# Kernel optimization log

Hardware: AMD Instinct MI355X
Metric: run time of the kernel (lower is better)

The kernel has to match this reference:

```python
import jax, jax.numpy as jnp
import numpy as np
import math

H = 16
SEG = 128
DIL = 2


def hilbert_perm(M: int) -> jnp.ndarray:
    # Boustrophedon (snake) traversal of a ceil(sqrt(M)) grid, matching
    # create_hilbert_mapping_simple: skip linear positions >= M, keep first M.
    g = int(math.ceil(math.sqrt(M)))
    grid = np.arange(g * g).reshape(g, g)
    grid[1::2] = grid[1::2, ::-1]
    flat = grid.reshape(-1)
    flat = flat[flat < M][:M]
    return jnp.asarray(flat, dtype=jnp.int32)


def setup_inputs() -> dict:
    key = jax.random.key(0)
    kx, kq, ko = jax.random.split(key, 3)
    B, M, D = 4, 4096, 1024
    x = jax.random.normal(kx, (B, M, D), dtype=jnp.float32)
    # nn.Linear weights: [out_features, in_features], y = x @ W.T
    w_qkv = jax.random.normal(kq, (3 * D, D), dtype=jnp.float32) * (D ** -0.5)
    w_out = jax.random.normal(ko, (D, D), dtype=jnp.float32) * (D ** -0.5)
    return {"x": x, "w_qkv": w_qkv, "w_out": w_out}


def reference(x, w_qkv, w_out):
    B, M, Dm = x.shape
    hd = Dm // H
    scale = hd ** -0.5
    S = M // SEG  # number of segments (M chosen as a multiple of SEG)

    qkv = x @ w_qkv.T                              # [B, M, 3*Dm]
    qkv = qkv.reshape(B, M, 3, H, hd)
    q = qkv[:, :, 0].transpose(0, 2, 1, 3)         # [B, H, M, hd]
    k = qkv[:, :, 1].transpose(0, 2, 1, 3)
    v = qkv[:, :, 2].transpose(0, 2, 1, 3)

    perm = hilbert_perm(M)
    qh = q[:, :, perm]                             # Hilbert-reordered
    kh = k[:, :, perm]
    vh = v[:, :, perm]

    # segment-local dilated attention: each query attends to keys at
    # positions seg_start + j*DIL within its own segment
    qh = qh.reshape(B, H, S, SEG, hd)
    kd = kh.reshape(B, H, S, SEG, hd)[:, :, :, ::DIL]   # [B,H,S,SEG//DIL,hd]
    vd = vh.reshape(B, H, S, SEG, hd)[:, :, :, ::DIL]

    scores = jnp.einsum('bhsqd,bhskd->bhsqk', qh * scale, kd)
    attn = jax.nn.softmax(scores, axis=-1)
    o = jnp.einsum('bhsqk,bhskd->bhsqd', attn, vd)       # [B,H,S,SEG,hd]
    o = o.reshape(B, H, M, hd).transpose(0, 2, 1, 3).reshape(B, M, Dm)
    return o @ w_out.T
```

## Files before the change

### kernel.cpp

```cpp
#include <hip/hip_runtime.h>


typedef _Float16 f16x8 __attribute__((ext_vector_type(8)));
typedef _Float16 f16x4 __attribute__((ext_vector_type(4)));
typedef float f32x4 __attribute__((ext_vector_type(4)));

__device__ __forceinline__ int hperm(int i) {
  int r = i >> 6, c = i & 63;
  return (r << 6) | ((r & 1) ? (63 - c) : c);
}
__device__ __forceinline__ int arow_gather(int mp) {
  int b = mp >> 11, i = mp & 2047;
  int s = i >> 6, j = i & 63;
  return b * 4096 + hperm(s * 128 + 2 * j);
}
__device__ __forceinline__ void gload_lds16(const _Float16* g, _Float16* l) {
  __builtin_amdgcn_global_load_lds(
      (const __attribute__((address_space(1))) void*)g,
      (__attribute__((address_space(3))) void*)l, 16, 0, 0);
}

__global__ __launch_bounds__(256) void cast_all(
    const float* __restrict__ x, _Float16* __restrict__ xh,
    const float* __restrict__ wq, _Float16* __restrict__ wqh,
    const float* __restrict__ wo, _Float16* __restrict__ woh) {
  for (int i = blockIdx.x * 256 + threadIdx.x; i < 5242880; i += 256 * 2048) {
    const float* s;
    _Float16* d;
    int j;
    if (i < 4194304) {
      s = x; d = xh; j = i;
    } else if (i < 4980736) {
      s = wq; d = wqh; j = i - 4194304;
    } else {
      s = wo; d = woh; j = i - 4980736;
    }
    float4 v = ((const float4*)s)[j];
    f16x4 o;
    o[0] = (_Float16)v.x;
    o[1] = (_Float16)v.y;
    o[2] = (_Float16)v.z;
    o[3] = (_Float16)v.w;
    *(f16x4*)&d[(size_t)j * 4] = o;
  }
}

#define BAR __builtin_amdgcn_s_barrier()
#define SB0 __builtin_amdgcn_sched_barrier(0)
#define LGKM_(n)                                                  \
  do {                                                            \
    asm volatile("s_waitcnt lgkmcnt(" #n ")" ::: "memory");       \
    SB0;                                                          \
  } while (0)
#define VM4 asm volatile("s_waitcnt vmcnt(4)" ::: "memory")
#define VM2 asm volatile("s_waitcnt vmcnt(2)" ::: "memory")
#define VM0 asm volatile("s_waitcnt vmcnt(0)" ::: "memory")
#define VMX

#define RDA(dst, bi, ks)                                       \
  _Pragma("unroll") for (int m = 0; m < 4; m++) dst[ks][m] =   \
      *(const f16x8*)(aRd[bi][ks] + m * 1024);
#define RDB(dst, bi, q)                                                     \
  _Pragma("unroll") for (int ks = 0; ks < 2; ks++)                          \
      _Pragma("unroll") for (int nf = 0; nf < 2; nf++) dst[ks][nf] =        \
          *(const f16x8*)(bRd[bi][ks] + (q)*2048 + nf * 1024);

#define SA(kt, buf, h)                                                        \
  do {                                                                        \
    gload_lds16(Ab + aOff[(h)*2] + (kt)*64, &lds[buf][0][(h)*8192 + t8]);     \
    gload_lds16(Ab + aOff[(h)*2 + 1] + (kt)*64,                               \
                &lds[buf][0][(h)*8192 + 4096 + t8]);                          \
  } while (0)
#define SBt(kt, buf, h)                                                       \
  do {                                                                        \
    gload_lds16(Bb + bOff[(h)*2] + (kt)*64, &lds[buf][1][(h)*8192 + t8]);     \
    gload_lds16(Bb + bOff[(h)*2 + 1] + (kt)*64,                               \
                &lds[buf][1][(h)*8192 + 4096 + t8]);                          \
  } while (0)

#define MMQ(AC, BS, q)                                                      \
  __builtin_amdgcn_s_setprio(1);                                            \
  _Pragma("unroll") for (int m = 0; m < 4; m++)                             \
      _Pragma("unroll") for (int nf = 0; nf < 2; nf++)                      \
          _Pragma("unroll") for (int ks = 0; ks < 2; ks++) acc[m][2 * (q) + \
                                                               nf] =        \
              __builtin_amdgcn_mfma_f32_16x16x32_f16(                       \
                  AC[ks][m], BS[ks][nf], acc[m][2 * (q) + nf], 0, 0, 0);    \
  __builtin_amdgcn_s_setprio(0);

#define KT(P, T, RD_A, S1, S2, S3, VQ2, VQ3, RD_B0, AN, AC, LGA, LGB3) \
  do {                                                                 \
                                                               \
    if (RD_A) { RDA(AN, (P) ^ 1, 0); }                                 \
    RDB(bS1, (P), 1);                                                  \
    if (S1) { SBt((T) + 1, (P) ^ 1, 1); }                              \
    BAR; LGKM_(LGA); MMQ(AC, bS0, 0);                                  \
                                                               \
    if (RD_A) { RDA(AN, (P) ^ 1, 1); }                                 \
    RDB(bS0, (P), 2);                                                  \
    if (S2) { SA((T) + 2, (P), 0); }                                   \
    BAR; LGKM_(LGA); MMQ(AC, bS1, 1);                                  \
                                                               \
    RDB(bS1, (P), 3);                                                  \
    if (S2) { SA((T) + 2, (P), 1); }                                   \
    VQ2; BAR; LGKM_(4); MMQ(AC, bS0, 2);                               \
                                                               \
    if (RD_B0) { RDB(bS0, (P) ^ 1, 0); }                               \
    if (S3) { SBt((T) + 2, (P), 0); }                                  \
    VQ3; BAR; LGKM_(LGB3); MMQ(AC, bS1, 3);                            \
  } while (0)

template <typename OutT>
__device__ __forceinline__ void gemm_body(
    const _Float16* __restrict__ Ab, const _Float16* __restrict__ Bb,
    const unsigned* aOff, const unsigned* bOff, OutT* __restrict__ C, int N,
    size_t arow0, size_t bcol0, _Float16 (&lds)[2][2][16384]) {
  const int t = threadIdx.x;
  const int lane = t & 63, wave = t >> 6;
  const int wm = wave >> 1, wn = wave & 1;
  const int lr = lane & 15, lg = lane >> 4;
  const int t8 = t * 8;

  const int cx0 = (lg * 8) ^ ((lr & 7) << 3);
  const int cx1 = cx0 ^ 32;
  const _Float16* aRd[2][2];
  const _Float16* bRd[2][2];
#pragma unroll
  for (int bf = 0; bf < 2; bf++) {
    aRd[bf][0] = &lds[bf][0][(wm * 64 + lr) * 64 + cx0];
    aRd[bf][1] = &lds[bf][0][(wm * 64 + lr) * 64 + cx1];
    bRd[bf][0] = &lds[bf][1][(wn * 128 + lr) * 64 + cx0];
    bRd[bf][1] = &lds[bf][1][(wn * 128 + lr) * 64 + cx1];
  }

  f32x4 acc[4][8] = {};
  f16x8 aEv[2][4], aOd[2][4], bS0[2][2], bS1[2][2];

  SA(0, 0, 0); SA(0, 0, 1); SBt(0, 0, 0); SBt(0, 0, 1);
  SA(1, 1, 0); SA(1, 1, 1);
  VM4;
  BAR;
  RDA(aEv, 0, 0); RDA(aEv, 0, 1); RDB(bS0, 0, 0);
  SBt(1, 1, 0);
  VM2;
  BAR;

  for (int i = 0; i < 7; i++) {
    KT(0, 2 * i,     1, 1, 1, 1, VM4, VM2, 1, aOd, aEv, 8, 4);
    KT(1, 2 * i + 1, 1, 1, 1, 1, VM4, VM2, 1, aEv, aOd, 8, 4);
  }
  KT(0, 14, 1, 1, 0, 0, VM0, VMX, 1, aOd, aEv, 8, 4);
  KT(1, 15, 0, 0, 0, 0, VMX, VMX, 0, aEv, aOd, 4, 0);

#pragma unroll
  for (int m = 0; m < 4; m++) {
    size_t row0 = arow0 + wm * 64 + m * 16 + lg * 4;
#pragma unroll
    for (int n = 0; n < 8; n++) {
      size_t col = bcol0 + wn * 128 + (n >> 1) * 32 + (n & 1) * 16 + lr;
#pragma unroll
      for (int j = 0; j < 4; j++)
        C[(row0 + j) * N + col] = (OutT)acc[m][n][j];
    }
  }
}

__global__ __launch_bounds__(512, 2) void gemm_qkv(
    const _Float16* __restrict__ xh, const _Float16* __restrict__ wqh,
    _Float16* __restrict__ qh, _Float16* __restrict__ kvh) {
  __shared__ _Float16 lds[2][2][16384];
  const int t = threadIdx.x;
  const int id = blockIdx.x;
  const int sw = (id & 7) * (gridDim.x >> 3) + (id >> 3);
  const bool iskv = sw >= 256;
  const int wid = iskv ? sw - 256 : sw;
  const int N = iskv ? 2048 : 1024;
  const int bn = iskv ? (wid & 7) : (wid & 3);
  const int bm = iskv ? (wid >> 3) : (wid >> 2);
  const _Float16* Bb = wqh + (iskv ? (size_t)1048576 : 0);
  _Float16* C = iskv ? kvh : qh;

  const int sgrow = t >> 3;
  const int sgcol = ((t & 7) * 8) ^ ((sgrow & 7) << 3);
  unsigned aOff[4], bOff[4];
#pragma unroll
  for (int r = 0; r < 4; r++) {
    int mr = bm * 256 + 64 * r + sgrow;
    int ar = iskv ? arow_gather(mr) : mr;
    aOff[r] = (unsigned)ar * 1024u + (unsigned)sgcol;
    bOff[r] = ((unsigned)(bn * 256 + 64 * r + sgrow)) * 1024u + (unsigned)sgcol;
  }
  gemm_body<_Float16>(xh, Bb, aOff, bOff, C, N, (size_t)bm * 256,
                      (size_t)bn * 256, lds);
}

__global__ __launch_bounds__(512, 2) void gemm_out(
    const _Float16* __restrict__ atth, const _Float16* __restrict__ woh,
    float* __restrict__ out) {
  __shared__ _Float16 lds[2][2][16384];
  const int t = threadIdx.x;
  const int id = blockIdx.x;
  const int sw = (id & 7) * (gridDim.x >> 3) + (id >> 3);
  const int bn = sw & 3, bm = sw >> 2;

  const int sgrow = t >> 3;
  const int sgcol = ((t & 7) * 8) ^ ((sgrow & 7) << 3);
  unsigned aOff[4], bOff[4];
#pragma unroll
  for (int r = 0; r < 4; r++) {
    aOff[r] = ((unsigned)(bm * 256 + 64 * r + sgrow)) * 1024u + (unsigned)sgcol;
    bOff[r] = ((unsigned)(bn * 256 + 64 * r + sgrow)) * 1024u + (unsigned)sgcol;
  }
  gemm_body<float>(atth, woh, aOff, bOff, out, 1024, (size_t)bm * 256,
                   (size_t)bn * 256, lds);
}

#define STRD 72

__global__ __launch_bounds__(256) void hilbert_attn(
    const _Float16* __restrict__ qh, const _Float16* __restrict__ kvh,
    _Float16* __restrict__ aout) {
  __shared__ _Float16 Qs[128 * STRD];
  __shared__ _Float16 Ks[64 * STRD];
  __shared__ _Float16 Vt[64 * STRD];
  __shared__ _Float16 Ps[128 * STRD];
  const int blk = blockIdx.x;
  const int s = blk & 31, h = (blk >> 5) & 15, b = blk >> 9;
  const int t = threadIdx.x, lane = t & 63, wave = t >> 6;
  const int lr = lane & 15, lg = lane >> 4, lk = lg * 8;
  const int col = (t & 7) * 8, rr = t >> 3;
  const size_t kvb = ((size_t)b * 2048 + s * 64) * 2048;

#pragma unroll
  for (int i = 0; i < 4; i++) {
    int m = i * 32 + rr;
    int p = b * 4096 + hperm(s * 128 + m);
    *(f16x8*)&Qs[m * STRD + col] =
        *(const f16x8*)&qh[(size_t)p * 1024 + h * 64 + col];
  }
#pragma unroll
  for (int i = 0; i < 2; i++) {
    int j = i * 32 + rr;
    *(f16x8*)&Ks[j * STRD + col] =
        *(const f16x8*)&kvh[kvb + (size_t)j * 2048 + h * 64 + col];
    f16x8 vv =
        *(const f16x8*)&kvh[kvb + (size_t)j * 2048 + 1024 + h * 64 + col];
#pragma unroll
    for (int e = 0; e < 8; e++) Vt[(col + e) * STRD + j] = vv[e];
  }
  __syncthreads();

  f32x4 accs[2][4] = {};
#pragma unroll
  for (int kk = 0; kk < 2; kk++) {
    f16x8 aa[2], bb[4];
#pragma unroll
    for (int m = 0; m < 2; m++)
      aa[m] = *(const f16x8*)&Qs[(wave * 32 + m * 16 + lr) * STRD + kk * 32 + lk];
#pragma unroll
    for (int n = 0; n < 4; n++)
      bb[n] = *(const f16x8*)&Ks[(n * 16 + lr) * STRD + kk * 32 + lk];
#pragma unroll
    for (int m = 0; m < 2; m++)
#pragma unroll
      for (int n = 0; n < 4; n++)
        accs[m][n] =
            __builtin_amdgcn_mfma_f32_16x16x32_f16(aa[m], bb[n], accs[m][n], 0, 0, 0);
  }

#pragma unroll
  for (int m = 0; m < 2; m++) {
#pragma unroll
    for (int j = 0; j < 4; j++) {
      float sc0 = accs[m][0][j] * 0.125f;
      float sc1 = accs[m][1][j] * 0.125f;
      float sc2 = accs[m][2][j] * 0.125f;
      float sc3 = accs[m][3][j] * 0.125f;
      float mx = fmaxf(fmaxf(sc0, sc1), fmaxf(sc2, sc3));
#pragma unroll
      for (int d = 1; d < 16; d <<= 1) mx = fmaxf(mx, __shfl_xor(mx, d, 16));
      float e0 = __expf(sc0 - mx), e1 = __expf(sc1 - mx);
      float e2 = __expf(sc2 - mx), e3 = __expf(sc3 - mx);
      float sum = (e0 + e1) + (e2 + e3);
#pragma unroll
      for (int d = 1; d < 16; d <<= 1) sum += __shfl_xor(sum, d, 16);
      float inv = 1.0f / sum;
      int row = wave * 32 + m * 16 + lg * 4 + j;
      Ps[row * STRD + 0 * 16 + lr] = (_Float16)(e0 * inv);
      Ps[row * STRD + 1 * 16 + lr] = (_Float16)(e1 * inv);
      Ps[row * STRD + 2 * 16 + lr] = (_Float16)(e2 * inv);
      Ps[row * STRD + 3 * 16 + lr] = (_Float16)(e3 * inv);
    }
  }
  __syncthreads();

  f32x4 acco[2][4] = {};
#pragma unroll
  for (int kk = 0; kk < 2; kk++) {
    f16x8 aa[2], bb[4];
#pragma unroll
    for (int m = 0; m < 2; m++)
      aa[m] = *(const f16x8*)&Ps[(wave * 32 + m * 16 + lr) * STRD + kk * 32 + lk];
#pragma unroll
    for (int n = 0; n < 4; n++)
      bb[n] = *(const f16x8*)&Vt[(n * 16 + lr) * STRD + kk * 32 + lk];
#pragma unroll
    for (int m = 0; m < 2; m++)
#pragma unroll
      for (int n = 0; n < 4; n++)
        acco[m][n] =
            __builtin_amdgcn_mfma_f32_16x16x32_f16(aa[m], bb[n], acco[m][n], 0, 0, 0);
  }

  const size_t orow0 = (size_t)b * 4096 + s * 128;
#pragma unroll
  for (int m = 0; m < 2; m++) {
#pragma unroll
    for (int n = 0; n < 4; n++) {
#pragma unroll
      for (int j = 0; j < 4; j++) {
        size_t row = orow0 + wave * 32 + m * 16 + lg * 4 + j;
        aout[row * 1024 + h * 64 + n * 16 + lr] = (_Float16)acco[m][n][j];
      }
    }
  }
}

extern "C" void kernel_launch(void* const* d_in, const int* in_sizes, int n_in,
                              void* d_out, int out_size, void* d_ws, size_t ws_size,
                              hipStream_t stream) {
  const float* x = (const float*)d_in[0];
  const float* w_qkv = (const float*)d_in[1];
  const float* w_out = (const float*)d_in[2];
  float* out = (float*)d_out;
  char* ws = (char*)d_ws;

  _Float16* xh = (_Float16*)(ws + 0);
  _Float16* wqh = (_Float16*)(ws + (size_t)33554432);
  _Float16* woh = (_Float16*)(ws + (size_t)39845888);
  _Float16* qh = (_Float16*)(ws + (size_t)41943040);
  _Float16* kvh = (_Float16*)(ws + (size_t)75497472);
  _Float16* atth = (_Float16*)(ws + (size_t)109051904);

  cast_all<<<2048, 256, 0, stream>>>(x, xh, w_qkv, wqh, w_out, woh);

  gemm_qkv<<<512, 512, 0, stream>>>(xh, wqh, qh, kvh);
  hilbert_attn<<<2048, 256, 0, stream>>>(qh, kvh, atth);
  gemm_out<<<256, 512, 0, stream>>>(atth, woh, out);
}
```

Before: 173.2 us.

## Shrink GEMM tiles to 256x128 and simplify the double-buffered pipeline

Shrinks the GEMM block tile from 256x256 to 256x128 and doubles the grid sizes for the QKV and output projections, so more workgroups fill the CUs (the output GEMM previously had only 256 blocks). The finely interleaved quarter-step pipeline is replaced by a simpler two-substep schedule with a full vmcnt(0) wait and a barrier per K tile. The trade-off is lower arithmetic intensity per block, more redundant A-tile loads, and less overlap of global loads with MFMA work.

```diff
diff --git a/kernel.cpp b/kernel.cpp
--- a/kernel.cpp
+++ b/kernel.cpp
@@ -47,74 +47,58 @@
 
 #define BAR __builtin_amdgcn_s_barrier()
 #define SB0 __builtin_amdgcn_sched_barrier(0)
-#define LGKM_(n)                                                  \
-  do {                                                            \
-    asm volatile("s_waitcnt lgkmcnt(" #n ")" ::: "memory");       \
-    SB0;                                                          \
+#define LGKM_(n)                                            \
+  do {                                                      \
+    asm volatile("s_waitcnt lgkmcnt(" #n ")" ::: "memory"); \
+    SB0;                                                    \
   } while (0)
-#define VM4 asm volatile("s_waitcnt vmcnt(4)" ::: "memory")
-#define VM2 asm volatile("s_waitcnt vmcnt(2)" ::: "memory")
+#define VM6 asm volatile("s_waitcnt vmcnt(6)" ::: "memory")
 #define VM0 asm volatile("s_waitcnt vmcnt(0)" ::: "memory")
-#define VMX
-
-#define RDA(dst, bi, ks)                                       \
-  _Pragma("unroll") for (int m = 0; m < 4; m++) dst[ks][m] =   \
-      *(const f16x8*)(aRd[bi][ks] + m * 1024);
-#define RDB(dst, bi, q)                                                     \
-  _Pragma("unroll") for (int ks = 0; ks < 2; ks++)                          \
-      _Pragma("unroll") for (int nf = 0; nf < 2; nf++) dst[ks][nf] =        \
-          *(const f16x8*)(bRd[bi][ks] + (q)*2048 + nf * 1024);
-
-#define SA(kt, buf, h)                                                        \
-  do {                                                                        \
-    gload_lds16(Ab + aOff[(h)*2] + (kt)*64, &lds[buf][0][(h)*8192 + t8]);     \
-    gload_lds16(Ab + aOff[(h)*2 + 1] + (kt)*64,                               \
-                &lds[buf][0][(h)*8192 + 4096 + t8]);                          \
+
+#define RDS(aset, bset, bufi, ks)                                          \
+  do {                                                                     \
+    _Pragma("unroll") for (int m = 0; m < 4; m++) aset[m] =                \
+        *(const f16x8*)(aRd[bufi][ks] + m * 1024);                         \
+    _Pragma("unroll") for (int n = 0; n < 4; n++) bset[n] =                \
+        *(const f16x8*)(bRd[bufi][ks] + n * 1024);                         \
   } while (0)
-#define SBt(kt, buf, h)                                                       \
-  do {                                                                        \
-    gload_lds16(Bb + bOff[(h)*2] + (kt)*64, &lds[buf][1][(h)*8192 + t8]);     \
-    gload_lds16(Bb + bOff[(h)*2 + 1] + (kt)*64,                               \
-                &lds[buf][1][(h)*8192 + 4096 + t8]);                          \
+
+#define STG6(kt, buf)                                                \
+  do {                                                               \
+    gload_lds16(Ab + aOff[0] + (kt)*64, &lds[buf][t8]);              \
+    gload_lds16(Ab + aOff[1] + (kt)*64, &lds[buf][4096 + t8]);       \
+    gload_lds16(Ab + aOff[2] + (kt)*64, &lds[buf][8192 + t8]);       \
+    gload_lds16(Ab + aOff[3] + (kt)*64, &lds[buf][12288 + t8]);      \
+    gload_lds16(Bb + bOff[0] + (kt)*64, &lds[buf][16384 + t8]);      \
+    gload_lds16(Bb + bOff[1] + (kt)*64, &lds[buf][20480 + t8]);      \
   } while (0)
 
-#define MMQ(AC, BS, q)                                                      \
-  __builtin_amdgcn_s_setprio(1);                                            \
-  _Pragma("unroll") for (int m = 0; m < 4; m++)                             \
-      _Pragma("unroll") for (int nf = 0; nf < 2; nf++)                      \
-          _Pragma("unroll") for (int ks = 0; ks < 2; ks++) acc[m][2 * (q) + \
-                                                               nf] =        \
-              __builtin_amdgcn_mfma_f32_16x16x32_f16(                       \
-                  AC[ks][m], BS[ks][nf], acc[m][2 * (q) + nf], 0, 0, 0);    \
+#define MM16(aset, bset)                                                   \
+  __builtin_amdgcn_s_setprio(1);                                           \
+  _Pragma("unroll") for (int m = 0; m < 4; m++)                            \
+      _Pragma("unroll") for (int n = 0; n < 4; n++) acc[m][n] =            \
+          __builtin_amdgcn_mfma_f32_16x16x32_f16(aset[m], bset[n],         \
+                                                 acc[m][n], 0, 0, 0);      \
   __builtin_amdgcn_s_setprio(0);
 
-#define KT(P, T, RD_A, S1, S2, S3, VQ2, VQ3, RD_B0, AN, AC, LGA, LGB3) \
-  do {                                                                 \
-                                                               \
-    if (RD_A) { RDA(AN, (P) ^ 1, 0); }                                 \
-    RDB(bS1, (P), 1);                                                  \
-    if (S1) { SBt((T) + 1, (P) ^ 1, 1); }                              \
-    BAR; LGKM_(LGA); MMQ(AC, bS0, 0);                                  \
-                                                               \
-    if (RD_A) { RDA(AN, (P) ^ 1, 1); }                                 \
-    RDB(bS0, (P), 2);                                                  \
-    if (S2) { SA((T) + 2, (P), 0); }                                   \
-    BAR; LGKM_(LGA); MMQ(AC, bS1, 1);                                  \
-                                                               \
-    RDB(bS1, (P), 3);                                                  \
-    if (S2) { SA((T) + 2, (P), 1); }                                   \
-    VQ2; BAR; LGKM_(4); MMQ(AC, bS0, 2);                               \
-                                                               \
-    if (RD_B0) { RDB(bS0, (P) ^ 1, 0); }                               \
-    if (S3) { SBt((T) + 2, (P), 0); }                                  \
-    VQ3; BAR; LGKM_(LGB3); MMQ(AC, bS1, 3);                            \
+#define TILE(P, T, DO_STG, DO_NEXT, LGB)   \
+  do {                                     \
+    RDS(a1, b1, P, 1);                     \
+    LGKM_(8);                              \
+    MM16(a0, b0);                          \
+    VM0;                                   \
+    BAR;                                   \
+    if (DO_NEXT) { RDS(a0, b0, (P) ^ 1, 0); } \
+    if (DO_STG) { STG6((T) + 2, P); }      \
+    LGKM_(LGB);                            \
+    MM16(a1, b1);                          \
   } while (0)
 
 template <typename OutT>
 __device__ __forceinline__ void gemm_body(
     const _Float16* __restrict__ Ab, const _Float16* __restrict__ Bb,
     const unsigned* aOff, const unsigned* bOff, OutT* __restrict__ C, int N,
-    size_t arow0, size_t bcol0, _Float16 (&lds)[2][2][16384]) {
+    size_t arow0, size_t bcol0, _Float16 (&lds)[2][24576]) {
   const int t = threadIdx.x;
   const int lane = t & 63, wave = t >> 6;
   const int wm = wave >> 1, wn = wave & 1;
@@ -127,37 +111,34 @@
   const _Float16* bRd[2][2];
 #pragma unroll
   for (int bf = 0; bf < 2; bf++) {
-    aRd[bf][0] = &lds[bf][0][(wm * 64 + lr) * 64 + cx0];
-    aRd[bf][1] = &lds[bf][0][(wm * 64 + lr) * 64 + cx1];
-    bRd[bf][0] = &lds[bf][1][(wn * 128 + lr) * 64 + cx0];
-    bRd[bf][1] = &lds[bf][1][(wn * 128 + lr) * 64 + cx1];
-  }
-
-  f32x4 acc[4][8] = {};
-  f16x8 aEv[2][4], aOd[2][4], bS0[2][2], bS1[2][2];
-
-  SA(0, 0, 0); SA(0, 0, 1); SBt(0, 0, 0); SBt(0, 0, 1);
-  SA(1, 1, 0); SA(1, 1, 1);
-  VM4;
+    aRd[bf][0] = &lds[bf][(wm * 64 + lr) * 64 + cx0];
+    aRd[bf][1] = &lds[bf][(wm * 64 + lr) * 64 + cx1];
+    bRd[bf][0] = &lds[bf][16384 + (wn * 64 + lr) * 64 + cx0];
+    bRd[bf][1] = &lds[bf][16384 + (wn * 64 + lr) * 64 + cx1];
+  }
+
+  f32x4 acc[4][4] = {};
+  f16x8 a0[4], b0[4], a1[4], b1[4];
+
+  STG6(0, 0);
+  STG6(1, 1);
+  VM6;
   BAR;
-  RDA(aEv, 0, 0); RDA(aEv, 0, 1); RDB(bS0, 0, 0);
-  SBt(1, 1, 0);
-  VM2;
-  BAR;
+  RDS(a0, b0, 0, 0);
 
   for (int i = 0; i < 7; i++) {
-    KT(0, 2 * i,     1, 1, 1, 1, VM4, VM2, 1, aOd, aEv, 8, 4);
-    KT(1, 2 * i + 1, 1, 1, 1, 1, VM4, VM2, 1, aEv, aOd, 8, 4);
-  }
-  KT(0, 14, 1, 1, 0, 0, VM0, VMX, 1, aOd, aEv, 8, 4);
-  KT(1, 15, 0, 0, 0, 0, VMX, VMX, 0, aEv, aOd, 4, 0);
+    TILE(0, 2 * i, 1, 1, 8);
+    TILE(1, 2 * i + 1, 1, 1, 8);
+  }
+  TILE(0, 14, 0, 1, 8);
+  TILE(1, 15, 0, 0, 0);
 
 #pragma unroll
   for (int m = 0; m < 4; m++) {
     size_t row0 = arow0 + wm * 64 + m * 16 + lg * 4;
 #pragma unroll
-    for (int n = 0; n < 8; n++) {
-      size_t col = bcol0 + wn * 128 + (n >> 1) * 32 + (n & 1) * 16 + lr;
+    for (int n = 0; n < 4; n++) {
+      size_t col = bcol0 + wn * 64 + n * 16 + lr;
 #pragma unroll
       for (int j = 0; j < 4; j++)
         C[(row0 + j) * N + col] = (OutT)acc[m][n][j];
@@ -168,51 +149,56 @@
 __global__ __launch_bounds__(512, 2) void gemm_qkv(
     const _Float16* __restrict__ xh, const _Float16* __restrict__ wqh,
     _Float16* __restrict__ qh, _Float16* __restrict__ kvh) {
-  __shared__ _Float16 lds[2][2][16384];
+  __shared__ _Float16 lds[2][24576];
   const int t = threadIdx.x;
   const int id = blockIdx.x;
   const int sw = (id & 7) * (gridDim.x >> 3) + (id >> 3);
-  const bool iskv = sw >= 256;
-  const int wid = iskv ? sw - 256 : sw;
+  const bool iskv = sw >= 512;
+  const int wid = sw & 511;
   const int N = iskv ? 2048 : 1024;
-  const int bn = iskv ? (wid & 7) : (wid & 3);
-  const int bm = iskv ? (wid >> 3) : (wid >> 2);
+  const int bn = iskv ? (wid & 15) : (wid & 7);
+  const int bm = iskv ? (wid >> 4) : (wid >> 3);
   const _Float16* Bb = wqh + (iskv ? (size_t)1048576 : 0);
   _Float16* C = iskv ? kvh : qh;
 
   const int sgrow = t >> 3;
   const int sgcol = ((t & 7) * 8) ^ ((sgrow & 7) << 3);
-  unsigned aOff[4], bOff[4];
+  unsigned aOff[4], bOff[2];
 #pragma unroll
   for (int r = 0; r < 4; r++) {
     int mr = bm * 256 + 64 * r + sgrow;
     int ar = iskv ? arow_gather(mr) : mr;
     aOff[r] = (unsigned)ar * 1024u + (unsigned)sgcol;
-    bOff[r] = ((unsigned)(bn * 256 + 64 * r + sgrow)) * 1024u + (unsigned)sgcol;
-  }
+  }
+#pragma unroll
+  for (int r = 0; r < 2; r++)
+    bOff[r] = ((unsigned)(bn * 128 + 64 * r + sgrow)) * 1024u + (unsigned)sgcol;
+
   gemm_body<_Float16>(xh, Bb, aOff, bOff, C, N, (size_t)bm * 256,
-                      (size_t)bn * 256, lds);
+                      (size_t)bn * 128, lds);
 }
 
 __global__ __launch_bounds__(512, 2) void gemm_out(
     const _Float16* __restrict__ atth, const _Float16* __restrict__ woh,
     float* __restrict__ out) {
-  __shared__ _Float16 lds[2][2][16384];
+  __shared__ _Float16 lds[2][24576];
   const int t = threadIdx.x;
   const int id = blockIdx.x;
   const int sw = (id & 7) * (gridDim.x >> 3) + (id >> 3);
-  const int bn = sw & 3, bm = sw >> 2;
+  const int bn = sw & 7, bm = sw >> 3;
 
   const int sgrow = t >> 3;
   const int sgcol = ((t & 7) * 8) ^ ((sgrow & 7) << 3);
-  unsigned aOff[4], bOff[4];
-#pragma unroll
-  for (int r = 0; r < 4; r++) {
+  unsigned aOff[4], bOff[2];
+#pragma unroll
+  for (int r = 0; r < 4; r++)
     aOff[r] = ((unsigned)(bm * 256 + 64 * r + sgrow)) * 1024u + (unsigned)sgcol;
-    bOff[r] = ((unsigned)(bn * 256 + 64 * r + sgrow)) * 1024u + (unsigned)sgcol;
-  }
+#pragma unroll
+  for (int r = 0; r < 2; r++)
+    bOff[r] = ((unsigned)(bn * 128 + 64 * r + sgrow)) * 1024u + (unsigned)sgcol;
+
   gemm_body<float>(atth, woh, aOff, bOff, out, 1024, (size_t)bm * 256,
-                   (size_t)bn * 256, lds);
+                   (size_t)bn * 128, lds);
 }
 
 #define STRD 72
@@ -344,7 +330,7 @@
 
   cast_all<<<2048, 256, 0, stream>>>(x, xh, w_qkv, wqh, w_out, woh);
 
-  gemm_qkv<<<512, 512, 0, stream>>>(xh, wqh, qh, kvh);
+  gemm_qkv<<<1024, 512, 0, stream>>>(xh, wqh, qh, kvh);
   hilbert_attn<<<2048, 256, 0, stream>>>(qh, kvh, atth);
-  gemm_out<<<256, 512, 0, stream>>>(atth, woh, out);
-}
+  gemm_out<<<512, 512, 0, stream>>>(atth, woh, out);
+}
```

Result: no change. 173.6 us (+0.2%).
